# Performance work log

Measured on AMD Instinct MI355X. Metric: run time of the kernel, lower is better.

Reference implementation:

```python
import jax, jax.numpy as jnp
import numpy as np

EPS = 1e-6
GRID_ORDER_K = 4
DIST_K = 3


def _smallest_k(d, k):
    # k smallest values along last axis, ascending (torch.topk largest=False)
    return -jax.lax.top_k(-d, k)[0]


def _radius_loss(real, fake):
    qs = jnp.array([0.05, 0.1, 0.25, 0.5, 0.75, 0.9, 0.95], jnp.float32)
    fq = jnp.quantile(fake[:, :, 2], qs)
    rq = jnp.quantile(real[:, :, 2], qs)
    return jnp.mean((fq - rq) ** 2)


def _grid_density_loss(real, fake):
    qs = jnp.array([0.05, 0.25, 0.5, 0.75, 0.95], jnp.float32)
    lx = jnp.mean((jnp.quantile(fake[:, :, 0], qs) - jnp.quantile(real[:, :, 0], qs)) ** 2)
    ly = jnp.mean((jnp.quantile(fake[:, :, 1], qs) - jnp.quantile(real[:, :, 1], qs)) ** 2)
    return (lx + ly) / 2


def _knn_dists_flat(x, k):
    # x: [B,N,3]; pairwise dist on xy with +eps under sqrt as in source
    xy = x[:, :, :2]
    d = jnp.sqrt(((xy[:, :, None, :] - xy[:, None, :, :]) ** 2).sum(-1) + EPS)  # [B,N,N]
    d = _smallest_k(d, k)  # [B,N,k]
    return d.reshape(x.shape[0], -1)


def _distance_loss(real, fake):
    qs = jnp.array([0.05, 0.5, 0.95], jnp.float32)
    rq = jnp.quantile(_knn_dists_flat(real, DIST_K), qs, axis=1)  # [3,B]
    fq = jnp.quantile(_knn_dists_flat(fake, DIST_K), qs, axis=1)
    return jnp.mean((fq - rq) ** 2)


def _hexatic_order(coords, k):
    # coords: [B,N,2] -> psi: [B,N] complex
    B, N, _ = coords.shape
    diffs = coords[:, :, None, :] - coords[:, None, :, :]  # [B,N,N,2]
    dx = diffs[..., 0]
    dx = dx + EPS * (jnp.abs(dx) < EPS).astype(dx.dtype)
    angles = jnp.arctan2(diffs[..., 1], dx)
    e_iktheta = jnp.exp(1j * k * angles)  # [B,N,N] complex64
    dist = jnp.sqrt((diffs ** 2).sum(-1) + EPS)
    eye = jnp.eye(N, dtype=bool)[None]
    dist = jnp.where(eye, jnp.inf, dist)
    kth = jax.lax.stop_gradient(_smallest_k(dist, k)[..., -1])  # [B,N]
    sigma = jnp.maximum(0.1 * jnp.maximum(kth[..., None], EPS), EPS)
    arg = jnp.clip((kth[..., None] - dist) / sigma, -50.0, 50.0)
    w = jax.nn.sigmoid(arg)
    psi = (e_iktheta * w).sum(2) / jnp.maximum(w.sum(2), EPS)
    return psi


def _grid_order_loss(samples):
    psi = _hexatic_order(samples[:, :, :2], GRID_ORDER_K)
    return -jnp.mean(jnp.sqrt(psi * jnp.conj(psi))).real


def _physical_feasibility_loss(fake):
    xy = fake[:, :, :2]
    r = fake[:, :, 2]
    N = fake.shape[1]
    sq = ((xy[:, :, None, :] - xy[:, None, :, :]) ** 2).sum(-1)
    d = jnp.sqrt(jnp.where(sq <= 0, 1.0, sq))  # safe sqrt (guard grads at 0)
    d = jnp.where(sq <= 0, 0.0, d)
    tril = jnp.tril(jnp.ones((N, N), bool))[None]
    d = jnp.where(tril, d, 0.0)
    d = jnp.where(d <= 0, jnp.inf, d)
    radii_pair = jnp.abs(r)[:, None, :] + jnp.abs(r)[:, :, None]
    overlap = jax.nn.relu(radii_pair - (d + 1e-4))  # sqrt(x**2)==x for x>=0
    return overlap.sum() / (radii_pair.sum() / 2)


def _gan_loss(fake_outputs):
    t = 0.9  # ones_like - 0.1 label smoothing
    logp = jnp.maximum(jnp.log(fake_outputs), -100.0)
    log1mp = jnp.maximum(jnp.log(1.0 - fake_outputs), -100.0)
    return -jnp.mean(t * logp + (1.0 - t) * log1mp)


def setup_inputs() -> dict:
    key = jax.random.key(0)
    k1, k2, k3 = jax.random.split(key, 3)
    B, N = 4, 2048
    real_images = jax.random.normal(k1, (B, N, 3), jnp.float32)
    fake_images = jax.random.normal(k2, (B, N, 3), jnp.float32)
    fake_outputs = jax.random.uniform(k3, (B, 1), jnp.float32, 1e-3, 1.0 - 1e-3)
    return {"real_images": real_images, "fake_images": fake_images, "fake_outputs": fake_outputs}


def reference(real_images, fake_images, fake_outputs):
    loss = _radius_loss(real_images, fake_images)
    loss = loss + _physical_feasibility_loss(fake_images)
    loss = loss + _gan_loss(fake_outputs)
    loss = loss + _grid_density_loss(real_images, fake_images)
    loss = loss + _distance_loss(real_images, fake_images)
    loss = loss + _grid_order_loss(fake_images)
    return loss
```

## Files before the change

### kernel.cpp

```cpp
#include <hip/hip_runtime.h>
#include <math.h>

#define B_SZ   4
#define N_PTS  2048
#define EPSF   1e-6f
#define CAP    768

#define WS_KNN_R 0
#define WS_KNN_F 24576
#define WS_FEAS  49152
#define WS_PSIP  50176
#define WS_RSUM  51200
#define WS_Q     51204
#define WS_TICK  51264
#define QZF (WS_Q + 0)
#define QZR (WS_Q + 7)
#define QXF (WS_Q + 14)
#define QXR (WS_Q + 19)
#define QYF (WS_Q + 24)
#define QYR (WS_Q + 29)
#define QDR (WS_Q + 34)
#define QDF (WS_Q + 46)
#define COMP_SCALE 256.0f
#define KNN_SCALE  1024.0f

__constant__ float c_qs7[7] = {0.05f, 0.1f, 0.25f, 0.5f, 0.75f, 0.9f, 0.95f};
__constant__ float c_qs5[5] = {0.05f, 0.25f, 0.5f, 0.75f, 0.95f};
__constant__ float c_qs3[3] = {0.05f, 0.5f, 0.95f};

#define CE(a, b) { float _lo = fminf(a, b), _hi = fmaxf(a, b); a = _lo; b = _hi; }

__device__ __forceinline__ void ins3a(float m[3], float v) {
    float h0 = fmaxf(m[0], v); m[0] = fminf(m[0], v);
    float h1 = fmaxf(m[1], h0); m[1] = fminf(m[1], h0);
    m[2] = fminf(m[2], h1);
}
__device__ __forceinline__ void ins5a(float m[5], float v) {
    float h0 = fmaxf(m[0], v); m[0] = fminf(m[0], v);
    float h1 = fmaxf(m[1], h0); m[1] = fminf(m[1], h0);
    float h2 = fmaxf(m[2], h1); m[2] = fminf(m[2], h1);
    float h3 = fmaxf(m[3], h2); m[3] = fminf(m[3], h2);
    m[4] = fminf(m[4], h3);
}

__global__ __launch_bounds__(256) void hs_pair_kernel(const float* __restrict__ real,
                                                      const float* __restrict__ fake,
                                                      float* __restrict__ ws) {
    __shared__ float2 sxy[N_PTS];
    __shared__ float sr[N_PTS];
    __shared__ float red[256];
    __shared__ unsigned short slist[4 * 2 * CAP];
    const int tid = threadIdx.x, wave = tid >> 6, lane = tid & 63;
    const int blk = blockIdx.x;
    if (blk == 0 && tid == 0) ((unsigned int*)ws)[WS_TICK] = 0u;

    if (blk < 1024) {
        const int b = blk >> 8, grp = blk & 255;
        const float* src = fake + (size_t)b * N_PTS * 3;
        for (int t = tid; t < N_PTS; t += 256) {
            const float* p = src + t * 3;
            sxy[t] = make_float2(p[0], p[1]);
            sr[t]  = fabsf(p[2]);
        }
        __syncthreads();
        const int p0 = grp * 8 + wave * 2;
        float px[2], py[2], pri[2], m[2][5];
#pragma unroll
        for (int t = 0; t < 2; ++t) {
            px[t] = sxy[p0 + t].x; py[t] = sxy[p0 + t].y;
            pri[t] = sr[p0 + t] - 1e-4f;
            m[t][0] = m[t][1] = m[t][2] = m[t][3] = m[t][4] = INFINITY;
        }
        float acc = 0.f;
        for (int j = lane; j < N_PTS; j += 64) {
            float2 q = sxy[j]; float br = sr[j];
#pragma unroll
            for (int t = 0; t < 2; ++t) {
                float dx = px[t] - q.x, dy = py[t] - q.y;
                float sq = fmaf(dx, dx, dy * dy);
                ins5a(m[t], sq);
                float ov = fmaxf((pri[t] + br) - sqrtf(sq), 0.f);
                acc += (sq > 0.f) ? ov : 0.f;
            }
        }
#pragma unroll
        for (int off = 1; off < 64; off <<= 1) {
#pragma unroll
            for (int t = 0; t < 2; ++t) {
                float b0 = __shfl_xor(m[t][0], off);
                float b1 = __shfl_xor(m[t][1], off);
                float b2 = __shfl_xor(m[t][2], off);
                float b3 = __shfl_xor(m[t][3], off);
                float b4 = __shfl_xor(m[t][4], off);
                float l0 = fminf(m[t][0], b4);
                float l1 = fminf(m[t][1], b3);
                float l2 = fminf(m[t][2], b2);
                float l3 = fminf(m[t][3], b1);
                float l4 = fminf(m[t][4], b0);
                CE(l0, l3); CE(l1, l4); CE(l0, l2); CE(l1, l3);
                CE(l0, l1); CE(l2, l4); CE(l1, l2); CE(l3, l4); CE(l2, l3);
                m[t][0] = l0; m[t][1] = l1; m[t][2] = l2; m[t][3] = l3; m[t][4] = l4;
            }
        }
        if (lane == 0) {
            float* kout = ws + WS_KNN_F + b * (N_PTS * 3);
#pragma unroll
            for (int t = 0; t < 2; ++t) {
                const int i = p0 + t;
                kout[i * 3 + 0] = sqrtf(m[t][0] + EPSF);
                kout[i * 3 + 1] = sqrtf(m[t][1] + EPSF);
                kout[i * 3 + 2] = sqrtf(m[t][2] + EPSF);
            }
        }
        float kth[2], invs[2], T2[2];
#pragma unroll
        for (int t = 0; t < 2; ++t) {
            kth[t] = sqrtf(m[t][4] + EPSF);
            const float sigma = fmaxf(0.1f * fmaxf(kth[t], EPSF), EPSF);
            invs[t] = 1.f / sigma;
            const float T = kth[t] + 50.f * sigma;
            T2[t] = T * T;
        }
        unsigned int cnt[2] = {0u, 0u};
        const int lbase = wave * 2 * CAP;
        for (int it = 0; it < 32; ++it) {
            const int j = it * 64 + lane;
            float2 q = sxy[j];
#pragma unroll
            for (int t = 0; t < 2; ++t) {
                float dx = px[t] - q.x, dy = py[t] - q.y;
                float sq = fmaf(dx, dx, dy * dy);
                const bool p = (sq <= T2[t]);
                const unsigned long long mk = __ballot(p);
                const unsigned int below = __builtin_amdgcn_mbcnt_hi(
                    (unsigned int)(mk >> 32),
                    __builtin_amdgcn_mbcnt_lo((unsigned int)mk, 0u));
                const unsigned int off = cnt[t] + below;
                if (p && off < CAP) slist[lbase + t * CAP + off] = (unsigned short)j;
                cnt[t] += (unsigned int)__popcll((long long)mk);
            }
        }
        float mypsi = 0.f;
#pragma unroll
        for (int t = 0; t < 2; ++t) {
            float swv = 0.f, srev = 0.f, simv = 0.f;
            if (cnt[t] <= CAP) {
                const int len = (int)cnt[t];
                for (int i = lane; i < len; i += 64) {
                    const int j = slist[lbase + t * CAP + i];
                    float2 q = sxy[j];
                    float dx = px[t] - q.x, dy = py[t] - q.y;
                    float sq = fmaf(dx, dx, dy * dy);
                    float dist = sqrtf(sq + EPSF);
                    dist = (j == p0 + t) ? INFINITY : dist;
                    float a = dx + ((fabsf(dx) < EPSF) ? EPSF : 0.f);
                    float arg = fminf(fmaxf((kth[t] - dist) * invs[t], -50.f), 50.f);
                    float e = __expf(-arg);
                    float w = __builtin_amdgcn_rcpf(1.f + e);
                    float aa = a * a, bb = dy * dy;
                    float n2 = aa + bb;
                    float z2r = aa - bb;
                    float t0 = a * dy; float z2i = t0 + t0;
                    float inv = __builtin_amdgcn_rcpf(n2);
                    float ur = z2r * inv, ui = z2i * inv;
                    float e4r = fmaf(ur, ur, -(ui * ui));
                    float t1 = ur * ui; float e4i = t1 + t1;
                    swv += w;
                    srev = fmaf(w, e4r, srev);
                    simv = fmaf(w, e4i, simv);
                }
            } else {
                for (int j = lane; j < N_PTS; j += 64) {
                    float2 q = sxy[j];
                    float dx = px[t] - q.x, dy = py[t] - q.y;
                    float sq = fmaf(dx, dx, dy * dy);
                    float dist = sqrtf(sq + EPSF);
                    dist = (j == p0 + t) ? INFINITY : dist;
                    float a = dx + ((fabsf(dx) < EPSF) ? EPSF : 0.f);
                    float arg = fminf(fmaxf((kth[t] - dist) * invs[t], -50.f), 50.f);
                    float e = __expf(-arg);
                    float w = __builtin_amdgcn_rcpf(1.f + e);
                    float aa = a * a, bb = dy * dy;
                    float n2 = aa + bb;
                    float z2r = aa - bb;
                    float t0 = a * dy; float z2i = t0 + t0;
                    float inv = __builtin_amdgcn_rcpf(n2);
                    float ur = z2r * inv, ui = z2i * inv;
                    float e4r = fmaf(ur, ur, -(ui * ui));
                    float t1 = ur * ui; float e4i = t1 + t1;
                    swv += w;
                    srev = fmaf(w, e4r, srev);
                    simv = fmaf(w, e4i, simv);
                }
            }
#pragma unroll
            for (int off = 1; off < 64; off <<= 1) {
                swv  += __shfl_xor(swv, off);
                srev += __shfl_xor(srev, off);
                simv += __shfl_xor(simv, off);
            }
            if (lane == 0) {
                const float den = fmaxf(swv, EPSF);
                const float pr = srev / den, pi = simv / den;
                mypsi += sqrtf(fmaf(pr, pr, pi * pi));
            }
        }
        red[tid] = acc;
        __syncthreads();
        for (int s = 128; s > 0; s >>= 1) {
            if (tid < s) red[tid] += red[tid + s];
            __syncthreads();
        }
        if (tid == 0) ws[WS_FEAS + blk] = red[0];
        __syncthreads();
        red[tid] = (lane == 0) ? mypsi : 0.f;
        __syncthreads();
        for (int s = 128; s > 0; s >>= 1) {
            if (tid < s) red[tid] += red[tid + s];
            __syncthreads();
        }
        if (tid == 0) ws[WS_PSIP + blk] = red[0];
        if (grp == 0) {
            __syncthreads();
            float rs = 0.f;
            for (int t = tid; t < N_PTS; t += 256) rs += sr[t];
            red[tid] = rs;
            __syncthreads();
            for (int s = 128; s > 0; s >>= 1) {
                if (tid < s) red[tid] += red[tid + s];
                __syncthreads();
            }
            if (tid == 0) ws[WS_RSUM + b] = red[0];
        }
    } else {
        const int rb = blk - 1024;
        const int b = rb >> 7, grp = rb & 127;
        const float* src = real + (size_t)b * N_PTS * 3;
        for (int t = tid; t < N_PTS; t += 256) {
            const float* p = src + t * 3;
            sxy[t] = make_float2(p[0], p[1]);
        }
        __syncthreads();
        const int p0 = grp * 16 + wave * 4;
        float px[4], py[4], m[4][3];
#pragma unroll
        for (int t = 0; t < 4; ++t) {
            px[t] = sxy[p0 + t].x; py[t] = sxy[p0 + t].y;
            m[t][0] = m[t][1] = m[t][2] = INFINITY;
        }
        for (int j = lane; j < N_PTS; j += 64) {
            float2 q = sxy[j];
#pragma unroll
            for (int t = 0; t < 4; ++t) {
                float dx = px[t] - q.x, dy = py[t] - q.y;
                float sq = fmaf(dx, dx, dy * dy);
                ins3a(m[t], sq);
            }
        }
#pragma unroll
        for (int off = 1; off < 64; off <<= 1) {
#pragma unroll
            for (int t = 0; t < 4; ++t) {
                float b0 = __shfl_xor(m[t][0], off);
                float b1 = __shfl_xor(m[t][1], off);
                float b2 = __shfl_xor(m[t][2], off);
                float l0 = fminf(m[t][0], b2);
                float l1 = fminf(m[t][1], b1);
                float l2 = fminf(m[t][2], b0);
                CE(l0, l1); CE(l0, l2); CE(l1, l2);
                m[t][0] = l0; m[t][1] = l1; m[t][2] = l2;
            }
        }
        if (lane == 0) {
            float* kout = ws + WS_KNN_R + b * (N_PTS * 3);
#pragma unroll
            for (int t = 0; t < 4; ++t) {
                const int i = p0 + t;
                kout[i * 3 + 0] = sqrtf(m[t][0] + EPSF);
                kout[i * 3 + 1] = sqrtf(m[t][1] + EPSF);
                kout[i * 3 + 2] = sqrtf(m[t][2] + EPSF);
            }
        }
    }
}

__global__ __launch_bounds__(256) void hs_quant_kernel(const float* __restrict__ real,
                                                       const float* __restrict__ fake,
                                                       const float* __restrict__ fouts,
                                                       float* __restrict__ ws,
                                                       float* __restrict__ out) {
    __shared__ unsigned int hist[4][4096];
    __shared__ unsigned int s_wsum[4];
    __shared__ float sred[256];
    __shared__ int s_last;
    unsigned int* wsu = (unsigned int*)ws;
    const int tid = threadIdx.x, wave = tid >> 6, lane = tid & 63;
    const int aid = blockIdx.x;

    const float* src; int step, n, nq, slot; float vlo, vw; const float* qs;
    if (aid < 6) {
        src = ((aid & 1) ? real : fake) + ((aid < 2) ? 2 : ((aid < 4) ? 0 : 1));
        step = 3; n = 8192;
        nq = (aid < 2) ? 7 : 5;
        slot = (aid < 2) ? (QZF + aid * 7) : (QXF + (aid - 2) * 5);
        vlo = -8.f; vw = 1.f / COMP_SCALE;
        qs = (aid < 2) ? c_qs7 : c_qs5;
    } else {
        const int a = aid - 6;
        src = ws + ((a < 4) ? WS_KNN_R + a * (N_PTS * 3) : WS_KNN_F + (a - 4) * (N_PTS * 3));
        step = 1; n = N_PTS * 3; nq = 3;
        slot = (a < 4) ? (QDR + a * 3) : (QDF + (a - 4) * 3);
        vlo = 0.f; vw = 1.f / KNN_SCALE;
        qs = c_qs3;
    }

    unsigned int* hflat = &hist[0][0];
#pragma unroll
    for (int i = 0; i < 64; ++i) hflat[i * 256 + tid] = 0u;
    __syncthreads();

    const float scale = (aid < 6) ? COMP_SCALE : KNN_SCALE;
    const float bias  = (aid < 6) ? 8.0f : 0.0f;
    for (int e = tid; e < n; e += 256) {
        const float v = src[(size_t)e * step];
        int bin = (int)floorf((v + bias) * scale);
        bin = (bin < 0) ? 0 : (bin > 4095 ? 4095 : bin);
        atomicAdd(&hist[wave][bin], 1u);
    }
    __syncthreads();

    unsigned int c[16], ps = 0;
    const int base = tid * 16;
#pragma unroll
    for (int i = 0; i < 16; ++i) {
        c[i] = hist[0][base + i] + hist[1][base + i] + hist[2][base + i] + hist[3][base + i];
        ps += c[i];
    }
    unsigned int incl = ps;
#pragma unroll
    for (int off = 1; off < 64; off <<= 1) {
        unsigned int nb = (unsigned int)__shfl_up((int)incl, off);
        if (lane >= off) incl += nb;
    }
    if (lane == 63) s_wsum[wave] = incl;
    __syncthreads();
    unsigned int woff = 0;
    for (int w2 = 0; w2 < wave; ++w2) woff += s_wsum[w2];
    unsigned int run = incl - ps + woff;
    unsigned int* sh_cum = &hist[0][0];
#pragma unroll
    for (int i = 0; i < 16; ++i) { run += c[i]; sh_cum[base + i] = run; }
    __syncthreads();

    if (tid < nq) {
        const float pos = qs[tid] * (float)(n - 1);
        const int k = (int)pos;
        const float frac = pos - (float)k;
        float v2[2];
#pragma unroll
        for (int t = 0; t < 2; ++t) {
            const unsigned int r = (unsigned int)(k + t);
            int lo_ = 0, hi_ = 4095;
            while (lo_ < hi_) {
                const int mid = (lo_ + hi_) >> 1;
                if (sh_cum[mid] > r) hi_ = mid; else lo_ = mid + 1;
            }
            const unsigned int excl = (lo_ > 0) ? sh_cum[lo_ - 1] : 0u;
            const unsigned int cnt  = sh_cum[lo_] - excl;
            v2[t] = vlo + ((float)lo_ + ((float)(r - excl) + 0.5f) / (float)cnt) * vw;
        }
        ws[slot + tid] = v2[0] + frac * (v2[1] - v2[0]);
    }

    __threadfence();
    __syncthreads();
    if (tid == 0) {
        const unsigned int t = atomicAdd(&wsu[WS_TICK], 1u);
        s_last = (t == 13u) ? 1 : 0;
    }
    __syncthreads();
    if (!s_last) return;
    __threadfence();

    float fs = 0.f, ps2 = 0.f;
    for (int t = tid; t < 1024; t += 256) {
        fs  += ws[WS_FEAS + t];
        ps2 += ws[WS_PSIP + t];
    }
    sred[tid] = fs;
    __syncthreads();
    for (int s = 128; s > 0; s >>= 1) {
        if (tid < s) sred[tid] += sred[tid + s];
        __syncthreads();
    }
    const float s_feas = sred[0];
    __syncthreads();
    sred[tid] = ps2;
    __syncthreads();
    for (int s = 128; s > 0; s >>= 1) {
        if (tid < s) sred[tid] += sred[tid + s];
        __syncthreads();
    }
    if (tid == 0) {
        const float psi_sum = sred[0];
        const float rsum = ws[WS_RSUM + 0] + ws[WS_RSUM + 1] + ws[WS_RSUM + 2] + ws[WS_RSUM + 3];
        float loss = 0.f;
        float sacc = 0.f;
        for (int qq = 0; qq < 7; ++qq) { float d = ws[QZF + qq] - ws[QZR + qq]; sacc += d * d; }
        loss += sacc / 7.f;
        loss += (0.5f * s_feas) / ((float)N_PTS * rsum);
        float g = 0.f;
        for (int b = 0; b < B_SZ; ++b) {
            float p = fouts[b];
            g += 0.9f * fmaxf(logf(p), -100.f) + 0.1f * fmaxf(logf(1.f - p), -100.f);
        }
        loss += -g / (float)B_SZ;
        float sx = 0.f, sy = 0.f;
        for (int qq = 0; qq < 5; ++qq) {
            float dx = ws[QXF + qq] - ws[QXR + qq]; sx += dx * dx;
            float dy = ws[QYF + qq] - ws[QYR + qq]; sy += dy * dy;
        }
        loss += 0.5f * (sx / 5.f + sy / 5.f);
        float sd = 0.f;
        for (int t = 0; t < 12; ++t) { float d = ws[QDF + t] - ws[QDR + t]; sd += d * d; }
        loss += sd / 12.f;
        loss += -psi_sum / (float)(B_SZ * N_PTS);
        out[0] = loss;
    }
}

extern "C" void kernel_launch(void* const* d_in, const int* in_sizes, int n_in,
                              void* d_out, int out_size, void* d_ws, size_t ws_size,
                              hipStream_t stream) {
    (void)in_sizes; (void)n_in; (void)out_size; (void)ws_size;
    const float* real  = (const float*)d_in[0];
    const float* fake  = (const float*)d_in[1];
    const float* fouts = (const float*)d_in[2];
    float* out = (float*)d_out;
    float* ws  = (float*)d_ws;

    hipLaunchKernelGGL(hs_pair_kernel,  dim3(1536), dim3(256), 0, stream, real, fake, ws);
    hipLaunchKernelGGL(hs_quant_kernel, dim3(14),   dim3(256), 0, stream, real, fake, fouts, ws, out);
}
```

Baseline: 111.9 us.

## Fuse pair and quantile kernels into one launch with per-batch completion tickets

```diff
diff --git a/kernel.cpp b/kernel.cpp
--- a/kernel.cpp
+++ b/kernel.cpp
@@ -12,7 +12,8 @@
 #define WS_PSIP  50176
 #define WS_RSUM  51200
 #define WS_Q     51204
-#define WS_TICK  51264
+#define WS_TICKC 51264
+#define WS_TICK2 51272
 #define QZF (WS_Q + 0)
 #define QZR (WS_Q + 7)
 #define QXF (WS_Q + 14)
@@ -21,8 +22,8 @@
 #define QYR (WS_Q + 29)
 #define QDR (WS_Q + 34)
 #define QDF (WS_Q + 46)
-#define COMP_SCALE 256.0f
-#define KNN_SCALE  1024.0f
+#define COMP_SCALE 128.0f
+#define KNN_SCALE  512.0f
 
 __constant__ float c_qs7[7] = {0.05f, 0.1f, 0.25f, 0.5f, 0.75f, 0.9f, 0.95f};
 __constant__ float c_qs5[5] = {0.05f, 0.25f, 0.5f, 0.75f, 0.95f};
@@ -43,37 +44,175 @@
     m[4] = fminf(m[4], h3);
 }
 
-__global__ __launch_bounds__(256) void hs_pair_kernel(const float* __restrict__ real,
-                                                      const float* __restrict__ fake,
-                                                      float* __restrict__ ws) {
-    __shared__ float2 sxy[N_PTS];
-    __shared__ float sr[N_PTS];
-    __shared__ float red[256];
-    __shared__ unsigned short slist[4 * 2 * CAP];
+union SmemU {
+    struct {
+        float2 sxy[N_PTS];
+        float  sr[N_PTS];
+        float  red[256];
+        unsigned short slist[4 * 2 * CAP];
+    } p1;
+    struct {
+        unsigned int hist[4][2048];
+        unsigned int swsum[4];
+        float sred[256];
+        int slast;
+    } p2;
+};
+
+__device__ __forceinline__ void quant_hist(SmemU& sm,
+                                           const float* __restrict__ src, int step, int n,
+                                           float bias, float scale,
+                                           const float* qs, int nq,
+                                           float vlo, float vw,
+                                           float* __restrict__ ws, int slot,
+                                           int tid, int wave, int lane) {
+    unsigned int* hflat = &sm.p2.hist[0][0];
+#pragma unroll
+    for (int i = 0; i < 32; ++i) hflat[i * 256 + tid] = 0u;
+    __syncthreads();
+    for (int e = tid; e < n; e += 256) {
+        const float v = src[(size_t)e * step];
+        int bin = (int)floorf((v + bias) * scale);
+        bin = (bin < 0) ? 0 : (bin > 2047 ? 2047 : bin);
+        atomicAdd(&sm.p2.hist[wave][bin], 1u);
+    }
+    __syncthreads();
+    unsigned int c[8], ps = 0;
+    const int base = tid * 8;
+#pragma unroll
+    for (int i = 0; i < 8; ++i) {
+        c[i] = sm.p2.hist[0][base + i] + sm.p2.hist[1][base + i]
+             + sm.p2.hist[2][base + i] + sm.p2.hist[3][base + i];
+        ps += c[i];
+    }
+    unsigned int incl = ps;
+#pragma unroll
+    for (int off = 1; off < 64; off <<= 1) {
+        unsigned int nb = (unsigned int)__shfl_up((int)incl, off);
+        if (lane >= off) incl += nb;
+    }
+    if (lane == 63) sm.p2.swsum[wave] = incl;
+    __syncthreads();
+    unsigned int woff = 0;
+    for (int w2 = 0; w2 < wave; ++w2) woff += sm.p2.swsum[w2];
+    unsigned int run = incl - ps + woff;
+#pragma unroll
+    for (int i = 0; i < 8; ++i) { run += c[i]; hflat[base + i] = run; }
+    __syncthreads();
+    if (tid < nq) {
+        const float pos = qs[tid] * (float)(n - 1);
+        const int k = (int)pos;
+        const float frac = pos - (float)k;
+        float v2[2];
+#pragma unroll
+        for (int t = 0; t < 2; ++t) {
+            const unsigned int r = (unsigned int)(k + t);
+            int lo_ = 0, hi_ = 2047;
+            while (lo_ < hi_) {
+                const int mid = (lo_ + hi_) >> 1;
+                if (hflat[mid] > r) hi_ = mid; else lo_ = mid + 1;
+            }
+            const unsigned int excl = (lo_ > 0) ? hflat[lo_ - 1] : 0u;
+            const unsigned int cnt  = hflat[lo_] - excl;
+            v2[t] = vlo + ((float)lo_ + ((float)(r - excl) + 0.5f) / (float)cnt) * vw;
+        }
+        ws[slot + tid] = v2[0] + frac * (v2[1] - v2[0]);
+    }
+    __syncthreads();
+}
+
+__device__ __forceinline__ void final_combine(SmemU& sm,
+                                              const float* __restrict__ fouts,
+                                              float* __restrict__ ws,
+                                              float* __restrict__ out, int tid) {
+    float fs = 0.f, ps2 = 0.f;
+    for (int t = tid; t < 1024; t += 256) {
+        fs  += ws[WS_FEAS + t];
+        ps2 += ws[WS_PSIP + t];
+    }
+    sm.p2.sred[tid] = fs;
+    __syncthreads();
+    for (int s = 128; s > 0; s >>= 1) {
+        if (tid < s) sm.p2.sred[tid] += sm.p2.sred[tid + s];
+        __syncthreads();
+    }
+    const float s_feas = sm.p2.sred[0];
+    __syncthreads();
+    sm.p2.sred[tid] = ps2;
+    __syncthreads();
+    for (int s = 128; s > 0; s >>= 1) {
+        if (tid < s) sm.p2.sred[tid] += sm.p2.sred[tid + s];
+        __syncthreads();
+    }
+    if (tid == 0) {
+        const float psi_sum = sm.p2.sred[0];
+        const float rsum = ws[WS_RSUM + 0] + ws[WS_RSUM + 1] + ws[WS_RSUM + 2] + ws[WS_RSUM + 3];
+        float loss = 0.f;
+        float sacc = 0.f;
+        for (int qq = 0; qq < 7; ++qq) { float d = ws[QZF + qq] - ws[QZR + qq]; sacc += d * d; }
+        loss += sacc / 7.f;
+        loss += (0.5f * s_feas) / ((float)N_PTS * rsum);
+        float g = 0.f;
+        for (int b = 0; b < B_SZ; ++b) {
+            float p = fouts[b];
+            g += 0.9f * fmaxf(logf(p), -100.f) + 0.1f * fmaxf(logf(1.f - p), -100.f);
+        }
+        loss += -g / (float)B_SZ;
+        float sx = 0.f, sy = 0.f;
+        for (int qq = 0; qq < 5; ++qq) {
+            float dx = ws[QXF + qq] - ws[QXR + qq]; sx += dx * dx;
+            float dy = ws[QYF + qq] - ws[QYR + qq]; sy += dy * dy;
+        }
+        loss += 0.5f * (sx / 5.f + sy / 5.f);
+        float sd = 0.f;
+        for (int t = 0; t < 12; ++t) { float d = ws[QDF + t] - ws[QDR + t]; sd += d * d; }
+        loss += sd / 12.f;
+        loss += -psi_sum / (float)(B_SZ * N_PTS);
+        out[0] = loss;
+    }
+}
+
+__global__ __launch_bounds__(256) void hs_fused_kernel(const float* __restrict__ real,
+                                                       const float* __restrict__ fake,
+                                                       const float* __restrict__ fouts,
+                                                       float* __restrict__ ws,
+                                                       float* __restrict__ out) {
+    __shared__ SmemU sm;
+    __shared__ unsigned int s_ticket;
+    unsigned int* wsu = (unsigned int*)ws;
     const int tid = threadIdx.x, wave = tid >> 6, lane = tid & 63;
     const int blk = blockIdx.x;
-    if (blk == 0 && tid == 0) ((unsigned int*)ws)[WS_TICK] = 0u;
-
-    if (blk < 1024) {
-        const int b = blk >> 8, grp = blk & 255;
+    if (blk == 0 && tid < 9) wsu[WS_TICKC + tid] = 0u;
+
+    if (blk < 6) {
+        const int aid = blk;
+        const float* src = ((aid & 1) ? real : fake) + ((aid < 2) ? 2 : ((aid < 4) ? 0 : 1));
+        const int nq = (aid < 2) ? 7 : 5;
+        const int slot = (aid < 2) ? (QZF + aid * 7) : (QXF + (aid - 2) * 5);
+        const float* qs = (aid < 2) ? c_qs7 : c_qs5;
+        quant_hist(sm, src, 3, 8192, 8.0f, COMP_SCALE, qs, nq,
+                   -8.0f, 1.0f / COMP_SCALE, ws, slot, tid, wave, lane);
+    } else if (blk < 1030) {
+        const int fb = blk - 6;
+        const int b = fb >> 8, grp = fb & 255;
         const float* src = fake + (size_t)b * N_PTS * 3;
         for (int t = tid; t < N_PTS; t += 256) {
             const float* p = src + t * 3;
-            sxy[t] = make_float2(p[0], p[1]);
-            sr[t]  = fabsf(p[2]);
+            sm.p1.sxy[t] = make_float2(p[0], p[1]);
+            sm.p1.sr[t]  = fabsf(p[2]);
         }
         __syncthreads();
         const int p0 = grp * 8 + wave * 2;
         float px[2], py[2], pri[2], m[2][5];
 #pragma unroll
         for (int t = 0; t < 2; ++t) {
-            px[t] = sxy[p0 + t].x; py[t] = sxy[p0 + t].y;
-            pri[t] = sr[p0 + t] - 1e-4f;
+            px[t] = sm.p1.sxy[p0 + t].x; py[t] = sm.p1.sxy[p0 + t].y;
+            pri[t] = sm.p1.sr[p0 + t] - 1e-4f;
             m[t][0] = m[t][1] = m[t][2] = m[t][3] = m[t][4] = INFINITY;
         }
         float acc = 0.f;
         for (int j = lane; j < N_PTS; j += 64) {
-            float2 q = sxy[j]; float br = sr[j];
+            float2 q = sm.p1.sxy[j]; float br = sm.p1.sr[j];
 #pragma unroll
             for (int t = 0; t < 2; ++t) {
                 float dx = px[t] - q.x, dy = py[t] - q.y;
@@ -125,7 +264,7 @@
         const int lbase = wave * 2 * CAP;
         for (int it = 0; it < 32; ++it) {
             const int j = it * 64 + lane;
-            float2 q = sxy[j];
+            float2 q = sm.p1.sxy[j];
 #pragma unroll
             for (int t = 0; t < 2; ++t) {
                 float dx = px[t] - q.x, dy = py[t] - q.y;
@@ -136,7 +275,7 @@
                     (unsigned int)(mk >> 32),
                     __builtin_amdgcn_mbcnt_lo((unsigned int)mk, 0u));
                 const unsigned int off = cnt[t] + below;
-                if (p && off < CAP) slist[lbase + t * CAP + off] = (unsigned short)j;
+                if (p && off < CAP) sm.p1.slist[lbase + t * CAP + off] = (unsigned short)j;
                 cnt[t] += (unsigned int)__popcll((long long)mk);
             }
         }
@@ -147,8 +286,8 @@
             if (cnt[t] <= CAP) {
                 const int len = (int)cnt[t];
                 for (int i = lane; i < len; i += 64) {
-                    const int j = slist[lbase + t * CAP + i];
-                    float2 q = sxy[j];
+                    const int j = sm.p1.slist[lbase + t * CAP + i];
+                    float2 q = sm.p1.sxy[j];
                     float dx = px[t] - q.x, dy = py[t] - q.y;
                     float sq = fmaf(dx, dx, dy * dy);
                     float dist = sqrtf(sq + EPSF);
@@ -171,7 +310,7 @@
                 }
             } else {
                 for (int j = lane; j < N_PTS; j += 64) {
-                    float2 q = sxy[j];
+                    float2 q = sm.p1.sxy[j];
                     float dx = px[t] - q.x, dy = py[t] - q.y;
                     float sq = fmaf(dx, dx, dy * dy);
                     float dist = sqrtf(sq + EPSF);
@@ -205,51 +344,59 @@
                 mypsi += sqrtf(fmaf(pr, pr, pi * pi));
             }
         }
-        red[tid] = acc;
+        sm.p1.red[tid] = acc;
         __syncthreads();
         for (int s = 128; s > 0; s >>= 1) {
-            if (tid < s) red[tid] += red[tid + s];
+            if (tid < s) sm.p1.red[tid] += sm.p1.red[tid + s];
             __syncthreads();
         }
-        if (tid == 0) ws[WS_FEAS + blk] = red[0];
-        __syncthreads();
-        red[tid] = (lane == 0) ? mypsi : 0.f;
+        if (tid == 0) ws[WS_FEAS + fb] = sm.p1.red[0];
+        __syncthreads();
+        sm.p1.red[tid] = (lane == 0) ? mypsi : 0.f;
         __syncthreads();
         for (int s = 128; s > 0; s >>= 1) {
-            if (tid < s) red[tid] += red[tid + s];
+            if (tid < s) sm.p1.red[tid] += sm.p1.red[tid + s];
             __syncthreads();
         }
-        if (tid == 0) ws[WS_PSIP + blk] = red[0];
+        if (tid == 0) ws[WS_PSIP + fb] = sm.p1.red[0];
         if (grp == 0) {
             __syncthreads();
             float rs = 0.f;
-            for (int t = tid; t < N_PTS; t += 256) rs += sr[t];
-            red[tid] = rs;
+            for (int t = tid; t < N_PTS; t += 256) rs += sm.p1.sr[t];
+            sm.p1.red[tid] = rs;
             __syncthreads();
             for (int s = 128; s > 0; s >>= 1) {
-                if (tid < s) red[tid] += red[tid + s];
+                if (tid < s) sm.p1.red[tid] += sm.p1.red[tid + s];
                 __syncthreads();
             }
-            if (tid == 0) ws[WS_RSUM + b] = red[0];
-        }
+            if (tid == 0) ws[WS_RSUM + b] = sm.p1.red[0];
+        }
+        __threadfence();
+        __syncthreads();
+        if (tid == 0) s_ticket = atomicAdd(&wsu[WS_TICKC + b], 1u);
+        __syncthreads();
+        if (s_ticket != 255u) return;
+        __threadfence();
+        quant_hist(sm, ws + WS_KNN_F + b * (N_PTS * 3), 1, N_PTS * 3, 0.0f, KNN_SCALE,
+                   c_qs3, 3, 0.0f, 1.0f / KNN_SCALE, ws, QDF + b * 3, tid, wave, lane);
     } else {
-        const int rb = blk - 1024;
+        const int rb = blk - 1030;
         const int b = rb >> 7, grp = rb & 127;
         const float* src = real + (size_t)b * N_PTS * 3;
         for (int t = tid; t < N_PTS; t += 256) {
             const float* p = src + t * 3;
-            sxy[t] = make_float2(p[0], p[1]);
+            sm.p1.sxy[t] = make_float2(p[0], p[1]);
         }
         __syncthreads();
         const int p0 = grp * 16 + wave * 4;
         float px[4], py[4], m[4][3];
 #pragma unroll
         for (int t = 0; t < 4; ++t) {
-            px[t] = sxy[p0 + t].x; py[t] = sxy[p0 + t].y;
+            px[t] = sm.p1.sxy[p0 + t].x; py[t] = sm.p1.sxy[p0 + t].y;
             m[t][0] = m[t][1] = m[t][2] = INFINITY;
         }
         for (int j = lane; j < N_PTS; j += 64) {
-            float2 q = sxy[j];
+            float2 q = sm.p1.sxy[j];
 #pragma unroll
             for (int t = 0; t < 4; ++t) {
                 float dx = px[t] - q.x, dy = py[t] - q.y;
@@ -281,152 +428,26 @@
                 kout[i * 3 + 2] = sqrtf(m[t][2] + EPSF);
             }
         }
-    }
-}
-
-__global__ __launch_bounds__(256) void hs_quant_kernel(const float* __restrict__ real,
-                                                       const float* __restrict__ fake,
-                                                       const float* __restrict__ fouts,
-                                                       float* __restrict__ ws,
-                                                       float* __restrict__ out) {
-    __shared__ unsigned int hist[4][4096];
-    __shared__ unsigned int s_wsum[4];
-    __shared__ float sred[256];
-    __shared__ int s_last;
-    unsigned int* wsu = (unsigned int*)ws;
-    const int tid = threadIdx.x, wave = tid >> 6, lane = tid & 63;
-    const int aid = blockIdx.x;
-
-    const float* src; int step, n, nq, slot; float vlo, vw; const float* qs;
-    if (aid < 6) {
-        src = ((aid & 1) ? real : fake) + ((aid < 2) ? 2 : ((aid < 4) ? 0 : 1));
-        step = 3; n = 8192;
-        nq = (aid < 2) ? 7 : 5;
-        slot = (aid < 2) ? (QZF + aid * 7) : (QXF + (aid - 2) * 5);
-        vlo = -8.f; vw = 1.f / COMP_SCALE;
-        qs = (aid < 2) ? c_qs7 : c_qs5;
-    } else {
-        const int a = aid - 6;
-        src = ws + ((a < 4) ? WS_KNN_R + a * (N_PTS * 3) : WS_KNN_F + (a - 4) * (N_PTS * 3));
-        step = 1; n = N_PTS * 3; nq = 3;
-        slot = (a < 4) ? (QDR + a * 3) : (QDF + (a - 4) * 3);
-        vlo = 0.f; vw = 1.f / KNN_SCALE;
-        qs = c_qs3;
-    }
-
-    unsigned int* hflat = &hist[0][0];
-#pragma unroll
-    for (int i = 0; i < 64; ++i) hflat[i * 256 + tid] = 0u;
-    __syncthreads();
-
-    const float scale = (aid < 6) ? COMP_SCALE : KNN_SCALE;
-    const float bias  = (aid < 6) ? 8.0f : 0.0f;
-    for (int e = tid; e < n; e += 256) {
-        const float v = src[(size_t)e * step];
-        int bin = (int)floorf((v + bias) * scale);
-        bin = (bin < 0) ? 0 : (bin > 4095 ? 4095 : bin);
-        atomicAdd(&hist[wave][bin], 1u);
-    }
-    __syncthreads();
-
-    unsigned int c[16], ps = 0;
-    const int base = tid * 16;
-#pragma unroll
-    for (int i = 0; i < 16; ++i) {
-        c[i] = hist[0][base + i] + hist[1][base + i] + hist[2][base + i] + hist[3][base + i];
-        ps += c[i];
-    }
-    unsigned int incl = ps;
-#pragma unroll
-    for (int off = 1; off < 64; off <<= 1) {
-        unsigned int nb = (unsigned int)__shfl_up((int)incl, off);
-        if (lane >= off) incl += nb;
-    }
-    if (lane == 63) s_wsum[wave] = incl;
-    __syncthreads();
-    unsigned int woff = 0;
-    for (int w2 = 0; w2 < wave; ++w2) woff += s_wsum[w2];
-    unsigned int run = incl - ps + woff;
-    unsigned int* sh_cum = &hist[0][0];
-#pragma unroll
-    for (int i = 0; i < 16; ++i) { run += c[i]; sh_cum[base + i] = run; }
-    __syncthreads();
-
-    if (tid < nq) {
-        const float pos = qs[tid] * (float)(n - 1);
-        const int k = (int)pos;
-        const float frac = pos - (float)k;
-        float v2[2];
-#pragma unroll
-        for (int t = 0; t < 2; ++t) {
-            const unsigned int r = (unsigned int)(k + t);
-            int lo_ = 0, hi_ = 4095;
-            while (lo_ < hi_) {
-                const int mid = (lo_ + hi_) >> 1;
-                if (sh_cum[mid] > r) hi_ = mid; else lo_ = mid + 1;
-            }
-            const unsigned int excl = (lo_ > 0) ? sh_cum[lo_ - 1] : 0u;
-            const unsigned int cnt  = sh_cum[lo_] - excl;
-            v2[t] = vlo + ((float)lo_ + ((float)(r - excl) + 0.5f) / (float)cnt) * vw;
-        }
-        ws[slot + tid] = v2[0] + frac * (v2[1] - v2[0]);
+        __threadfence();
+        __syncthreads();
+        if (tid == 0) s_ticket = atomicAdd(&wsu[WS_TICKC + 4 + b], 1u);
+        __syncthreads();
+        if (s_ticket != 127u) return;
+        __threadfence();
+        quant_hist(sm, ws + WS_KNN_R + b * (N_PTS * 3), 1, N_PTS * 3, 0.0f, KNN_SCALE,
+                   c_qs3, 3, 0.0f, 1.0f / KNN_SCALE, ws, QDR + b * 3, tid, wave, lane);
     }
 
     __threadfence();
     __syncthreads();
     if (tid == 0) {
-        const unsigned int t = atomicAdd(&wsu[WS_TICK], 1u);
-        s_last = (t == 13u) ? 1 : 0;
-    }
-    __syncthreads();
-    if (!s_last) return;
+        const unsigned int t2 = atomicAdd(&wsu[WS_TICK2], 1u);
+        sm.p2.slast = (t2 == 13u) ? 1 : 0;
+    }
+    __syncthreads();
+    if (!sm.p2.slast) return;
     __threadfence();
-
-    float fs = 0.f, ps2 = 0.f;
-    for (int t = tid; t < 1024; t += 256) {
-        fs  += ws[WS_FEAS + t];
-        ps2 += ws[WS_PSIP + t];
-    }
-    sred[tid] = fs;
-    __syncthreads();
-    for (int s = 128; s > 0; s >>= 1) {
-        if (tid < s) sred[tid] += sred[tid + s];
-        __syncthreads();
-    }
-    const float s_feas = sred[0];
-    __syncthreads();
-    sred[tid] = ps2;
-    __syncthreads();
-    for (int s = 128; s > 0; s >>= 1) {
-        if (tid < s) sred[tid] += sred[tid + s];
-        __syncthreads();
-    }
-    if (tid == 0) {
-        const float psi_sum = sred[0];
-        const float rsum = ws[WS_RSUM + 0] + ws[WS_RSUM + 1] + ws[WS_RSUM + 2] + ws[WS_RSUM + 3];
-        float loss = 0.f;
-        float sacc = 0.f;
-        for (int qq = 0; qq < 7; ++qq) { float d = ws[QZF + qq] - ws[QZR + qq]; sacc += d * d; }
-        loss += sacc / 7.f;
-        loss += (0.5f * s_feas) / ((float)N_PTS * rsum);
-        float g = 0.f;
-        for (int b = 0; b < B_SZ; ++b) {
-            float p = fouts[b];
-            g += 0.9f * fmaxf(logf(p), -100.f) + 0.1f * fmaxf(logf(1.f - p), -100.f);
-        }
-        loss += -g / (float)B_SZ;
-        float sx = 0.f, sy = 0.f;
-        for (int qq = 0; qq < 5; ++qq) {
-            float dx = ws[QXF + qq] - ws[QXR + qq]; sx += dx * dx;
-            float dy = ws[QYF + qq] - ws[QYR + qq]; sy += dy * dy;
-        }
-        loss += 0.5f * (sx / 5.f + sy / 5.f);
-        float sd = 0.f;
-        for (int t = 0; t < 12; ++t) { float d = ws[QDF + t] - ws[QDR + t]; sd += d * d; }
-        loss += sd / 12.f;
-        loss += -psi_sum / (float)(B_SZ * N_PTS);
-        out[0] = loss;
-    }
+    final_combine(sm, fouts, ws, out, tid);
 }
 
 extern "C" void kernel_launch(void* const* d_in, const int* in_sizes, int n_in,
@@ -439,6 +460,5 @@
     float* out = (float*)d_out;
     float* ws  = (float*)d_ws;
 
-    hipLaunchKernelGGL(hs_pair_kernel,  dim3(1536), dim3(256), 0, stream, real, fake, ws);
-    hipLaunchKernelGGL(hs_quant_kernel, dim3(14),   dim3(256), 0, stream, real, fake, fouts, ws, out);
-}
+    hipLaunchKernelGGL(hs_fused_kernel, dim3(1542), dim3(256), 0, stream, real, fake, fouts, ws, out);
+}
```

Result: slower. 197.6 us (+76.6%).
